# Performance work log

Hardware: AMD Instinct MI355X
Metric: run time of the kernel (lower is better)

## Reference

```python
import jax, jax.numpy as jnp
import numpy as np

Z, K, H, Y = 128, 256, 512, 4  # z_size, key_size, hidden_size, y_dim


def setup_inputs() -> dict:
    key = jax.random.key(0)
    ks = jax.random.split(key, 8)
    B, T, P = 512, 32, 32
    s = lambda k, shape, sc: (jax.random.normal(k, shape, jnp.float32) * sc)
    return {
        "x_seq": jax.random.normal(ks[0], (B, T, P, P), jnp.float32),
        "W_enc": s(ks[1], (P * P, Z), 0.03),
        "gamma": jnp.ones((Z,), jnp.float32),
        "beta": jnp.zeros((Z,), jnp.float32),
        "W_ih": s(ks[2], (4 * H, K + 1), 0.05),
        "W_hh": s(ks[3], (4 * H, H), 0.04),
        "b_ih": jnp.zeros((4 * H,), jnp.float32),
        "b_hh": jnp.zeros((4 * H,), jnp.float32),
        "W_key": s(ks[4], (K, H), 0.06),
        "b_key": jnp.zeros((K,), jnp.float32),
        "W_g": s(ks[5], (1, H), 0.06),
        "b_g": jnp.zeros((1,), jnp.float32),
        "conf_gain": jnp.ones((1,), jnp.float32),
        "conf_bias": jnp.zeros((1,), jnp.float32),
        "W_y": s(ks[6], (Y, H), 0.06),
        "b_y": jnp.zeros((Y,), jnp.float32),
    }


def _lstm_cell(x, h, c, W_ih, W_hh, b_ih, b_hh):
    # PyTorch gate order: i, f, g, o
    gates = x @ W_ih.T + b_ih + h @ W_hh.T + b_hh
    i, f, g, o = jnp.split(gates, 4, axis=-1)
    c = jax.nn.sigmoid(f) * c + jax.nn.sigmoid(i) * jnp.tanh(g)
    h = jax.nn.sigmoid(o) * jnp.tanh(c)
    return h, c


def _forward(x_seq, W_enc, gamma, beta, W_ih, W_hh, b_ih, b_hh,
             W_key, b_key, W_g, b_g, conf_gain, conf_bias, W_y, b_y):
    B, T, P, _ = x_seq.shape
    # encoder: flatten -> linear to z_size (stand-in for Encoder_mlp)
    z = x_seq.reshape(B, T, P * P) @ W_enc  # [B, T, Z]
    # context norm over the sequence dim (single task segment)
    mu = z.mean(axis=1, keepdims=True)
    sig = jnp.sqrt(z.var(axis=1, keepdims=True) + 1e-8)
    z = (z - mu) / sig * gamma + beta

    M = T + 1  # T+1 steps; final step feeds a zero z_t
    z_pad = jnp.concatenate([z, jnp.zeros((B, 1, Z), z.dtype)], axis=1)  # [B, M, Z]

    h0 = jnp.zeros((B, H), z.dtype)
    c0 = jnp.zeros((B, H), z.dtype)
    kr0 = jnp.zeros((B, K + 1), z.dtype)
    Mk0 = jnp.zeros((B, M, K), z.dtype)
    Mv0 = jnp.zeros((B, M, Z), z.dtype)

    def step(carry, t):
        h, c, key_r, M_k, M_v = carry
        z_t = jax.lax.dynamic_index_in_dim(z_pad, t, axis=1, keepdims=False)  # [B, Z]
        h, c = _lstm_cell(key_r, h, c, W_ih, W_hh, b_ih, b_hh)
        key_w = jax.nn.relu(h @ W_key.T + b_key)          # [B, K]
        g = jax.nn.sigmoid(h @ W_g.T + b_g)               # [B, 1]
        y_lin = h @ W_y.T + b_y                            # [B, Y]
        # attention read over valid memory slots j < t
        scores = jnp.einsum('bz,bmz->bm', z_t, M_v)        # [B, M]
        valid = (jnp.arange(M) < t)[None, :]
        w_k = jax.nn.softmax(jnp.where(valid, scores, -1e9), axis=1)
        c_k = jax.nn.sigmoid(scores * conf_gain + conf_bias)
        kv = jnp.concatenate([M_k, c_k[..., None]], axis=2)  # [B, M, K+1]
        attn = g * jnp.einsum('bm,bmd->bd', w_k, kv)          # [B, K+1]
        key_r_new = jnp.where(t == 0, jnp.zeros_like(attn), attn)
        # append to memory at slot t
        M_k = jax.lax.dynamic_update_slice_in_dim(M_k, key_w[:, None, :], t, axis=1)
        M_v = jax.lax.dynamic_update_slice_in_dim(M_v, z_t[:, None, :], t, axis=1)
        return (h, c, key_r_new, M_k, M_v), y_lin

    _, ys = jax.lax.scan(step, (h0, c0, kr0, Mk0, Mv0), jnp.arange(M))
    return ys[-1]  # y_pred_linear from final step, [B, Y]


def reference(x_seq, W_enc, gamma, beta, W_ih, W_hh, b_ih, b_hh,
              W_key, b_key, W_g, b_g, conf_gain, conf_bias, W_y, b_y):
    y_pred_linear = _forward(x_seq, W_enc, gamma, beta, W_ih, W_hh, b_ih, b_hh,
                             W_key, b_key, W_g, b_g, conf_gain, conf_bias, W_y, b_y)
    y_pred = jnp.argmax(y_pred_linear, axis=1)
    return y_pred_linear, y_pred
```

## Files before the change

kernel.cpp:

```cpp
#include <hip/hip_runtime.h>
#include <math.h>

typedef unsigned short ushort;
typedef unsigned int uint;
typedef __bf16 bf16x8 __attribute__((ext_vector_type(8)));
typedef float f32x4 __attribute__((ext_vector_type(4)));

#define ZS    128
#define KS    256
#define HS    512
#define BATCH 512
#define TT    32
#define MM    33
#define NB    2304
#define KPAD  800
#define HOFF  272
#define LDA   800

static __device__ __forceinline__ float sigf(float x) { return 1.f / (1.f + expf(-x)); }
static __device__ __forceinline__ float bf2f(ushort u) { return __uint_as_float((uint)u << 16); }

__global__ void prep_w(const float* __restrict__ W_ih, const float* __restrict__ W_hh,
                       const float* __restrict__ W_key, const float* __restrict__ b_ih,
                       const float* __restrict__ b_hh, const float* __restrict__ b_key,
                       const float* __restrict__ W_enc,
                       ushort* __restrict__ Whi, ushort* __restrict__ Wlo,
                       ushort* __restrict__ Behi, ushort* __restrict__ Belo,
                       float* __restrict__ biasN)
{
    int idx = blockIdx.x * 256 + threadIdx.x;
    if (idx < NB) {
        float bv;
        if (idx < 2048) { int j = idx >> 2, gi = idx & 3, r = gi * 512 + j; bv = b_ih[r] + b_hh[r]; }
        else bv = b_key[idx - 2048];
        biasN[idx] = bv;
    }
    if (idx < NB * KPAD) {
        int n = idx / KPAD, k = idx - n * KPAD;
        float v = 0.f;
        if (n < 2048) {
            int j = n >> 2, gi = n & 3, r = gi * 512 + j;
            if (k < 257) v = W_ih[r * 257 + k];
            else if (k >= HOFF && k < HOFF + 512) v = W_hh[r * 512 + (k - HOFF)];
        } else {
            if (k >= HOFF && k < HOFF + 512) v = W_key[(n - 2048) * 512 + (k - HOFF)];
        }
        uint u = __float_as_uint(v);
        Whi[idx] = (ushort)(u >> 16);
        float lo = v - __uint_as_float(u & 0xFFFF0000u);
        Wlo[idx] = (ushort)(__float_as_uint(lo) >> 16);
    } else if (idx < NB * KPAD + 128 * 1024) {
        int e = idx - NB * KPAD;
        int n = e >> 10, k = e & 1023;
        float v = W_enc[k * 128 + n];
        uint u = __float_as_uint(v);
        Behi[e] = (ushort)(u >> 16);
        float lo = v - __uint_as_float(u & 0xFFFF0000u);
        Belo[e] = (ushort)(__float_as_uint(lo) >> 16);
    }
}

__global__ __launch_bounds__(256, 4)
void gemm_enc(const float* __restrict__ A,
              const ushort* __restrict__ Bhi, const ushort* __restrict__ Blo,
              float* __restrict__ out)
{
    constexpr int BN = 128, NI = 4;
    constexpr int AHI = 0, ALO = 32 * 40, BHI = 64 * 40, BLO = 64 * 40 + BN * 40;
    constexpr int BUF = 64 * 40 + 2 * BN * 40;
    __shared__ ushort lds[2 * BUF];
    const int tid = threadIdx.x;
    const int row0 = blockIdx.x * 32, n0 = 0;
    const int lda = 1024, ldb = 1024, nslice = 32;
    const int l = tid & 63, w = tid >> 6, wm = w >> 1, wn = w & 1;
    const int lm = l & 15, kg = (l >> 4) << 3;

    f32x4 acc[NI];
    const f32x4 zero4 = {0.f, 0.f, 0.f, 0.f};
#pragma unroll
    for (int ni = 0; ni < NI; ni++) acc[ni] = zero4;

    float4 avf;
    uint4 bhv[BN / 64], blv[BN / 64];

    auto LOADG = [&](int s) {
        const int k0 = s * 32;
        int r = tid >> 3, c = (tid & 7) << 2;
        avf = *(const float4*)(A + (size_t)(row0 + r) * lda + k0 + c);
#pragma unroll
        for (int i = 0; i < BN / 64; i++) {
            int idx = tid + 256 * i, r2 = idx >> 2, c2 = (idx & 3) << 3;
            bhv[i] = *(const uint4*)(Bhi + (size_t)(n0 + r2) * ldb + k0 + c2);
            blv[i] = *(const uint4*)(Blo + (size_t)(n0 + r2) * ldb + k0 + c2);
        }
    };
    auto STORE = [&](int buf) {
        ushort* L = lds + buf * BUF;
        int r = tid >> 3, c = (tid & 7) << 2;
        uint u0 = __float_as_uint(avf.x), u1 = __float_as_uint(avf.y);
        uint u2 = __float_as_uint(avf.z), u3 = __float_as_uint(avf.w);
        uint hp0 = (u1 & 0xFFFF0000u) | (u0 >> 16);
        uint hp1 = (u3 & 0xFFFF0000u) | (u2 >> 16);
        float l0 = avf.x - __uint_as_float(u0 & 0xFFFF0000u);
        float l1 = avf.y - __uint_as_float(u1 & 0xFFFF0000u);
        float l2 = avf.z - __uint_as_float(u2 & 0xFFFF0000u);
        float l3 = avf.w - __uint_as_float(u3 & 0xFFFF0000u);
        uint lp0 = (__float_as_uint(l1) & 0xFFFF0000u) | (__float_as_uint(l0) >> 16);
        uint lp1 = (__float_as_uint(l3) & 0xFFFF0000u) | (__float_as_uint(l2) >> 16);
        *(uint2*)&L[AHI + r * 40 + c] = make_uint2(hp0, hp1);
        *(uint2*)&L[ALO + r * 40 + c] = make_uint2(lp0, lp1);
#pragma unroll
        for (int i = 0; i < BN / 64; i++) {
            int idx = tid + 256 * i, r2 = idx >> 2, c2 = (idx & 3) << 3;
            *(uint4*)&L[BHI + r2 * 40 + c2] = bhv[i];
            *(uint4*)&L[BLO + r2 * 40 + c2] = blv[i];
        }
    };
    auto COMPUTE = [&](int buf) {
        const ushort* L = lds + buf * BUF;
        bf16x8 ah, alv, bh[NI], bl[NI];
        {
            int r = wm * 16 + lm;
            ah  = *(const bf16x8*)&L[AHI + r * 40 + kg];
            alv = *(const bf16x8*)&L[ALO + r * 40 + kg];
        }
#pragma unroll
        for (int ni = 0; ni < NI; ni++) {
            int r = wn * (BN / 2) + ni * 16 + lm;
            bh[ni] = *(const bf16x8*)&L[BHI + r * 40 + kg];
            bl[ni] = *(const bf16x8*)&L[BLO + r * 40 + kg];
        }
#pragma unroll
        for (int ni = 0; ni < NI; ni++) {
            acc[ni] = __builtin_amdgcn_mfma_f32_16x16x32_bf16(ah,  bh[ni], acc[ni], 0, 0, 0);
            acc[ni] = __builtin_amdgcn_mfma_f32_16x16x32_bf16(ah,  bl[ni], acc[ni], 0, 0, 0);
            acc[ni] = __builtin_amdgcn_mfma_f32_16x16x32_bf16(alv, bh[ni], acc[ni], 0, 0, 0);
        }
    };

    LOADG(0);
    STORE(0);
    for (int s = 0; s < nslice; s++) {
        __syncthreads();
        if (s + 1 < nslice) LOADG(s + 1);
        COMPUTE(s & 1);
        if (s + 1 < nslice) STORE((s + 1) & 1);
    }

    const int crow = (l >> 4) << 2;
#pragma unroll
    for (int ni = 0; ni < NI; ni++)
#pragma unroll
        for (int r = 0; r < 4; r++) {
            int m = row0 + wm * 16 + crow + r;
            int z = n0 + wn * (BN / 2) + ni * 16 + lm;
            out[(size_t)(m >> 5) * (MM * ZS) + (m & 31) * ZS + z] = acc[ni][r];
        }
}

__global__ __launch_bounds__(256, 4)
void gemm_step(const ushort* __restrict__ Ahi, const ushort* __restrict__ Alo,
               const ushort* __restrict__ Whi, const ushort* __restrict__ Wlo,
               float* __restrict__ P0, float* __restrict__ P1)
{
    constexpr int AHI = 0, ALO = 64 * 40, BHI = 128 * 40, BLO = 192 * 40;
    constexpr int BUF = 256 * 40;
    __shared__ ushort lds[2 * BUF];
    const int tid = threadIdx.x;
    int wg = blockIdx.x;
    int swz = (wg & 7) * 72 + (wg >> 3);
    int zz = swz / 288;
    int rr = swz - zz * 288;
    const int bx = rr >> 3, by = rr & 7;
    const int kb = zz ? 13 : 0, kc = zz ? 12 : 13;
    float* __restrict__ out = zz ? P1 : P0;
    const int row0 = by * 64, n0 = bx * 64;
    const int l = tid & 63, w = tid >> 6, wm = w >> 1, wn = w & 1;
    const int lm = l & 15, kg = (l >> 4) << 3;
    const int ar = tid >> 2, ac = (tid & 3) << 3;

    f32x4 acc[2][2];
    const f32x4 zero4 = {0.f, 0.f, 0.f, 0.f};
    acc[0][0] = zero4; acc[0][1] = zero4; acc[1][0] = zero4; acc[1][1] = zero4;

    uint4 av0, av1, bv0, bv1;

    auto LOADG = [&](int a) {
        const int k0 = a * 32;
        av0 = *(const uint4*)(Ahi + (size_t)(row0 + ar) * LDA + k0 + ac);
        av1 = *(const uint4*)(Alo + (size_t)(row0 + ar) * LDA + k0 + ac);
        bv0 = *(const uint4*)(Whi + (size_t)(n0 + ar) * KPAD + k0 + ac);
        bv1 = *(const uint4*)(Wlo + (size_t)(n0 + ar) * KPAD + k0 + ac);
    };
    auto STORE = [&](int buf) {
        ushort* L = lds + buf * BUF;
        int off = ar * 40 + ac;
        *(uint4*)&L[AHI + off] = av0;
        *(uint4*)&L[ALO + off] = av1;
        *(uint4*)&L[BHI + off] = bv0;
        *(uint4*)&L[BLO + off] = bv1;
    };
    auto COMPUTE = [&](int buf) {
        const ushort* L = lds + buf * BUF;
        bf16x8 ah[2], al[2], bh[2], bl[2];
#pragma unroll
        for (int mi = 0; mi < 2; mi++) {
            int r = wm * 32 + mi * 16 + lm;
            ah[mi] = *(const bf16x8*)&L[AHI + r * 40 + kg];
            al[mi] = *(const bf16x8*)&L[ALO + r * 40 + kg];
        }
#pragma unroll
        for (int ni = 0; ni < 2; ni++) {
            int r = wn * 32 + ni * 16 + lm;
            bh[ni] = *(const bf16x8*)&L[BHI + r * 40 + kg];
            bl[ni] = *(const bf16x8*)&L[BLO + r * 40 + kg];
        }
#pragma unroll
        for (int mi = 0; mi < 2; mi++)
#pragma unroll
            for (int ni = 0; ni < 2; ni++) {
                acc[mi][ni] = __builtin_amdgcn_mfma_f32_16x16x32_bf16(ah[mi], bh[ni], acc[mi][ni], 0, 0, 0);
                acc[mi][ni] = __builtin_amdgcn_mfma_f32_16x16x32_bf16(ah[mi], bl[ni], acc[mi][ni], 0, 0, 0);
                acc[mi][ni] = __builtin_amdgcn_mfma_f32_16x16x32_bf16(al[mi], bh[ni], acc[mi][ni], 0, 0, 0);
            }
    };

    LOADG(kb);
    STORE(0);
    for (int s = 0; s < kc; s++) {
        __syncthreads();
        if (s + 1 < kc) LOADG(kb + s + 1);
        COMPUTE(s & 1);
        if (s + 1 < kc) STORE((s + 1) & 1);
    }

    const int crow = (l >> 4) << 2;
#pragma unroll
    for (int mi = 0; mi < 2; mi++)
#pragma unroll
        for (int ni = 0; ni < 2; ni++)
#pragma unroll
            for (int r = 0; r < 4; r++) {
                int b = row0 + wm * 32 + mi * 16 + crow + r;
                int n = n0 + wn * 32 + ni * 16 + lm;
                out[(size_t)b * NB + n] = acc[mi][ni][r];
            }
}

__global__ __launch_bounds__(256)
void cell_k(const float* __restrict__ P0, const float* __restrict__ P1,
            const float* __restrict__ biasN, float* __restrict__ cst,
            ushort* __restrict__ outHi, ushort* __restrict__ outLo,
            float* __restrict__ Mk,
            const float* __restrict__ W_g, const float* __restrict__ b_g,
            const float* __restrict__ watt, const float* __restrict__ wc,
            int t)
{
    __shared__ float hsh[512];
    __shared__ float red[256];
    __shared__ float wts[32];
    __shared__ float gsh;
    int b = blockIdx.x, tid = threadIdx.x;
    const float* p0 = P0 + (size_t)b * NB;
    const float* p1 = P1 + (size_t)b * NB;
    ushort* rHi = outHi + (size_t)b * LDA;
    ushort* rLo = outLo + (size_t)b * LDA;
#pragma unroll
    for (int u = 0; u < 2; u++) {
        int j = tid + u * 256;
        float4 a  = *(const float4*)(p0 + 4 * j);
        float4 c4 = *(const float4*)(p1 + 4 * j);
        float4 bb = *(const float4*)(biasN + 4 * j);
        float gi = a.x + c4.x + bb.x;
        float gf = a.y + c4.y + bb.y;
        float gg = a.z + c4.z + bb.z;
        float go = a.w + c4.w + bb.w;
        float iv = sigf(gi), fv = sigf(gf), gv = tanhf(gg), ov = sigf(go);
        float cn = fv * cst[(size_t)b * HS + j] + iv * gv;
        float hv = ov * tanhf(cn);
        cst[(size_t)b * HS + j] = cn;
        hsh[j] = hv;
        uint uu = __float_as_uint(hv);
        rHi[HOFF + j] = (ushort)(uu >> 16);
        float lo = hv - __uint_as_float(uu & 0xFFFF0000u);
        rLo[HOFF + j] = (ushort)(__float_as_uint(lo) >> 16);
    }
    float kv = fmaxf(p0[2048 + tid] + p1[2048 + tid] + biasN[2048 + tid], 0.f);
    if (t >= 1) Mk[((size_t)(t - 1) * BATCH + b) * KS + tid] = kv;
    if (t < 1 || t > 31) return;
    if (tid < t) wts[tid] = watt[(b * MM + t) * MM + tid];
    __syncthreads();
    red[tid] = hsh[tid] * W_g[tid] + hsh[tid + 256] * W_g[tid + 256];
    __syncthreads();
    for (int s = 128; s > 0; s >>= 1) {
        if (tid < s) red[tid] += red[tid + s];
        __syncthreads();
    }
    if (tid == 0) gsh = sigf(red[0] + b_g[0]);
    __syncthreads();
    float g = gsh;
    float acc = wts[t - 1] * kv;
    for (int m = 0; m < t - 1; m++)
        acc += wts[m] * Mk[((size_t)m * BATCH + b) * KS + tid];
    float v = g * acc;
    uint u2 = __float_as_uint(v);
    rHi[tid] = (ushort)(u2 >> 16);
    float lo2 = v - __uint_as_float(u2 & 0xFFFF0000u);
    rLo[tid] = (ushort)(__float_as_uint(lo2) >> 16);
    if (tid == 0) {
        float vc = g * wc[b * MM + t];
        uint uc = __float_as_uint(vc);
        rHi[256] = (ushort)(uc >> 16);
        float lc = vc - __uint_as_float(uc & 0xFFFF0000u);
        rLo[256] = (ushort)(__float_as_uint(lc) >> 16);
    }
}

__global__ void norm_k(float* __restrict__ z_pad, const float* __restrict__ gamma,
                       const float* __restrict__ beta)
{
    int b = blockIdx.x, zc = threadIdx.x;
    float* zb = z_pad + (size_t)b * (MM * ZS);
    float s = 0.f, s2 = 0.f;
    for (int t = 0; t < TT; t++) { float v = zb[t * ZS + zc]; s += v; s2 += v * v; }
    float mu = s * (1.f / 32.f);
    float var = s2 * (1.f / 32.f) - mu * mu;
    float rstd = 1.f / sqrtf(var + 1e-8f);
    float ga = gamma[zc], be = beta[zc];
    for (int t = 0; t < TT; t++) {
        float v = zb[t * ZS + zc];
        zb[t * ZS + zc] = (v - mu) * rstd * ga + be;
    }
    zb[TT * ZS + zc] = 0.f;
}

__global__ __launch_bounds__(256)
void scores_k(const float* __restrict__ z_pad, const float* __restrict__ cg_p,
              const float* __restrict__ cb_p, float* __restrict__ watt,
              float* __restrict__ wc)
{
    __shared__ float zs[MM * 129];
    int b = blockIdx.x, tid = threadIdx.x;
    const float* zb = z_pad + (size_t)b * (MM * ZS);
    for (int i = tid; i < MM * ZS; i += 256) {
        int m = i >> 7, k = i & 127;
        zs[m * 129 + k] = zb[i];
    }
    __syncthreads();
    float cg = cg_p[0], cb = cb_p[0];
    int wid = tid >> 6, lane = tid & 63;
    for (int t = 1 + wid; t <= 32; t += 4) {
        int m = lane;
        float s = -3.0e38f;
        if (m < t) {
            const float* zt = &zs[t * 129];
            const float* zm = &zs[m * 129];
            float acc = 0.f;
#pragma unroll 8
            for (int k = 0; k < ZS; k++) acc += zt[k] * zm[k];
            s = acc;
        }
        float mx = s;
        for (int off = 1; off < 64; off <<= 1) mx = fmaxf(mx, __shfl_xor(mx, off));
        float e = (m < t) ? expf(s - mx) : 0.f;
        float sum = e;
        for (int off = 1; off < 64; off <<= 1) sum += __shfl_xor(sum, off);
        float w = e / sum;
        if (m < t) watt[(b * MM + t) * MM + m] = w;
        float p = (m < t) ? w * sigf(s * cg + cb) : 0.f;
        for (int off = 1; off < 64; off <<= 1) p += __shfl_xor(p, off);
        if (lane == 0) wc[b * MM + t] = p;
    }
}

__global__ void y_k(const ushort* __restrict__ inpHi, const ushort* __restrict__ inpLo,
                    const float* __restrict__ W_y, const float* __restrict__ b_y,
                    float* __restrict__ out)
{
    int b = blockIdx.x, lane = threadIdx.x;
    const ushort* hHi = inpHi + (size_t)b * LDA + HOFF;
    const ushort* hLo = inpLo + (size_t)b * LDA + HOFF;
    float a0 = 0, a1 = 0, a2 = 0, a3 = 0;
    for (int r = 0; r < 8; r++) {
        int k = lane + r * 64;
        float hv = bf2f(hHi[k]) + bf2f(hLo[k]);
        a0 += hv * W_y[k];
        a1 += hv * W_y[512 + k];
        a2 += hv * W_y[1024 + k];
        a3 += hv * W_y[1536 + k];
    }
    for (int off = 32; off > 0; off >>= 1) {
        a0 += __shfl_xor(a0, off);
        a1 += __shfl_xor(a1, off);
        a2 += __shfl_xor(a2, off);
        a3 += __shfl_xor(a3, off);
    }
    if (lane == 0) {
        float y0 = a0 + b_y[0], y1 = a1 + b_y[1], y2 = a2 + b_y[2], y3 = a3 + b_y[3];
        out[b * 4 + 0] = y0; out[b * 4 + 1] = y1; out[b * 4 + 2] = y2; out[b * 4 + 3] = y3;
        int best = 0; float bv = y0;
        if (y1 > bv) { bv = y1; best = 1; }
        if (y2 > bv) { bv = y2; best = 2; }
        if (y3 > bv) { bv = y3; best = 3; }
        out[2048 + b] = (float)best;
    }
}

extern "C" void kernel_launch(void* const* d_in, const int* in_sizes, int n_in,
                              void* d_out, int out_size, void* d_ws, size_t ws_size,
                              hipStream_t stream)
{
    const float* x_seq = (const float*)d_in[0];
    const float* W_enc = (const float*)d_in[1];
    const float* gamma = (const float*)d_in[2];
    const float* beta  = (const float*)d_in[3];
    const float* W_ih  = (const float*)d_in[4];
    const float* W_hh  = (const float*)d_in[5];
    const float* b_ih  = (const float*)d_in[6];
    const float* b_hh  = (const float*)d_in[7];
    const float* W_key = (const float*)d_in[8];
    const float* b_key = (const float*)d_in[9];
    const float* W_g   = (const float*)d_in[10];
    const float* b_g   = (const float*)d_in[11];
    const float* cgain = (const float*)d_in[12];
    const float* cbias = (const float*)d_in[13];
    const float* W_y   = (const float*)d_in[14];
    const float* b_y   = (const float*)d_in[15];

    float* ws    = (float*)d_ws;
    float* z_pad = ws;
    float* watt  = z_pad + 2162688;
    float* wcv   = watt + 557568;
    float* Mk    = wcv + 16896;
    float* biasN = Mk + 4194304;
    float* cst   = biasN + 2304;
    ushort* inpHi0 = (ushort*)(cst + 262144);
    ushort* inpLo0 = inpHi0 + 409600;
    ushort* inpHi1 = inpLo0 + 409600;
    ushort* inpLo1 = inpHi1 + 409600;
    ushort* Whi  = inpLo1 + 409600;
    ushort* Wlo  = Whi + NB * KPAD;
    ushort* Behi = Wlo + NB * KPAD;
    ushort* Belo = Behi + 131072;
    float* P0 = (float*)(Belo + 131072);
    float* P1 = P0 + (size_t)BATCH * NB;

    hipMemsetAsync(cst, 0, 262144 * sizeof(float) + 4 * 409600 * sizeof(ushort), stream);

    prep_w<<<(NB * KPAD + 131072 + 255) / 256, 256, 0, stream>>>(
        W_ih, W_hh, W_key, b_ih, b_hh, b_key, W_enc, Whi, Wlo, Behi, Belo, biasN);

    gemm_enc<<<512, 256, 0, stream>>>(x_seq, Behi, Belo, z_pad);
    norm_k<<<512, 128, 0, stream>>>(z_pad, gamma, beta);
    scores_k<<<512, 256, 0, stream>>>(z_pad, cgain, cbias, watt, wcv);

    for (int t = 0; t <= 32; t++) {
        ushort* inHiC = (t & 1) ? inpHi1 : inpHi0;
        ushort* inLoC = (t & 1) ? inpLo1 : inpLo0;
        ushort* inHiN = (t & 1) ? inpHi0 : inpHi1;
        ushort* inLoN = (t & 1) ? inpLo0 : inpLo1;
        gemm_step<<<576, 256, 0, stream>>>(inHiC, inLoC, Whi, Wlo, P0, P1);
        cell_k<<<512, 256, 0, stream>>>(P0, P1, biasN, cst, inHiN, inLoN,
                                        Mk, W_g, b_g, watt, wcv, t);
    }
    y_k<<<512, 64, 0, stream>>>(inpHi1, inpLo1, W_y, b_y, (float*)d_out);
}
```

Baseline: 942.0 us.

## Fuse LSTM cell epilogue into per-step GEMM with single-wave 32x32 tiles

The per-step GEMM now uses one-wave 32x32 tiles that read operands straight from global memory, with no LDS staging and no split-K into P0/P1 partials. Its epilogue applies the bias and LSTM gate nonlinearities (or the ReLU key output) directly and writes h/c and the memory keys. A slimmer post kernel handles the gate scalar and the attention read, and it is skipped at steps where it does nothing. This removes the partial-sum round trip through global memory and part of each step's launch work, at the cost of losing LDS reuse and relying on cache hits for repeated operand loads. The post kernel rebuilds h from the hi/lo bf16 split rather than fp32, a small accuracy change.

```diff
diff --git a/kernel.cpp b/kernel.cpp
--- a/kernel.cpp
+++ b/kernel.cpp
@@ -158,63 +158,47 @@
         }
 }
 
-__global__ __launch_bounds__(256, 4)
+__global__ __launch_bounds__(64, 2)
 void gemm_step(const ushort* __restrict__ Ahi, const ushort* __restrict__ Alo,
                const ushort* __restrict__ Whi, const ushort* __restrict__ Wlo,
-               float* __restrict__ P0, float* __restrict__ P1)
-{
-    constexpr int AHI = 0, ALO = 64 * 40, BHI = 128 * 40, BLO = 192 * 40;
-    constexpr int BUF = 256 * 40;
-    __shared__ ushort lds[2 * BUF];
+               const float* __restrict__ biasN, float* __restrict__ cst,
+               ushort* __restrict__ outHi, ushort* __restrict__ outLo,
+               float* __restrict__ Mk, int t)
+{
+    __shared__ float eps[32 * 33];
     const int tid = threadIdx.x;
     int wg = blockIdx.x;
-    int swz = (wg & 7) * 72 + (wg >> 3);
-    int zz = swz / 288;
-    int rr = swz - zz * 288;
-    const int bx = rr >> 3, by = rr & 7;
-    const int kb = zz ? 13 : 0, kc = zz ? 12 : 13;
-    float* __restrict__ out = zz ? P1 : P0;
-    const int row0 = by * 64, n0 = bx * 64;
-    const int l = tid & 63, w = tid >> 6, wm = w >> 1, wn = w & 1;
-    const int lm = l & 15, kg = (l >> 4) << 3;
-    const int ar = tid >> 2, ac = (tid & 3) << 3;
+    int swz = (wg & 7) * 144 + (wg >> 3);
+    const int bx = swz >> 4, by = swz & 15;
+    const int row0 = by * 32, n0 = bx * 32;
+    const int lm = tid & 15, kg = (tid >> 4) << 3;
+    const int crow = (tid >> 4) << 2;
 
     f32x4 acc[2][2];
     const f32x4 zero4 = {0.f, 0.f, 0.f, 0.f};
     acc[0][0] = zero4; acc[0][1] = zero4; acc[1][0] = zero4; acc[1][1] = zero4;
 
-    uint4 av0, av1, bv0, bv1;
-
-    auto LOADG = [&](int a) {
-        const int k0 = a * 32;
-        av0 = *(const uint4*)(Ahi + (size_t)(row0 + ar) * LDA + k0 + ac);
-        av1 = *(const uint4*)(Alo + (size_t)(row0 + ar) * LDA + k0 + ac);
-        bv0 = *(const uint4*)(Whi + (size_t)(n0 + ar) * KPAD + k0 + ac);
-        bv1 = *(const uint4*)(Wlo + (size_t)(n0 + ar) * KPAD + k0 + ac);
-    };
-    auto STORE = [&](int buf) {
-        ushort* L = lds + buf * BUF;
-        int off = ar * 40 + ac;
-        *(uint4*)&L[AHI + off] = av0;
-        *(uint4*)&L[ALO + off] = av1;
-        *(uint4*)&L[BHI + off] = bv0;
-        *(uint4*)&L[BLO + off] = bv1;
-    };
-    auto COMPUTE = [&](int buf) {
-        const ushort* L = lds + buf * BUF;
+    const ushort* pA0h = Ahi + (size_t)(row0 + lm) * LDA + kg;
+    const ushort* pA1h = Ahi + (size_t)(row0 + 16 + lm) * LDA + kg;
+    const ushort* pA0l = Alo + (size_t)(row0 + lm) * LDA + kg;
+    const ushort* pA1l = Alo + (size_t)(row0 + 16 + lm) * LDA + kg;
+    const ushort* pB0h = Whi + (size_t)(n0 + lm) * KPAD + kg;
+    const ushort* pB1h = Whi + (size_t)(n0 + 16 + lm) * KPAD + kg;
+    const ushort* pB0l = Wlo + (size_t)(n0 + lm) * KPAD + kg;
+    const ushort* pB1l = Wlo + (size_t)(n0 + 16 + lm) * KPAD + kg;
+
+#pragma unroll
+    for (int s = 0; s < 25; s++) {
+        const int k0 = s * 32;
         bf16x8 ah[2], al[2], bh[2], bl[2];
-#pragma unroll
-        for (int mi = 0; mi < 2; mi++) {
-            int r = wm * 32 + mi * 16 + lm;
-            ah[mi] = *(const bf16x8*)&L[AHI + r * 40 + kg];
-            al[mi] = *(const bf16x8*)&L[ALO + r * 40 + kg];
-        }
-#pragma unroll
-        for (int ni = 0; ni < 2; ni++) {
-            int r = wn * 32 + ni * 16 + lm;
-            bh[ni] = *(const bf16x8*)&L[BHI + r * 40 + kg];
-            bl[ni] = *(const bf16x8*)&L[BLO + r * 40 + kg];
-        }
+        ah[0] = *(const bf16x8*)(pA0h + k0);
+        ah[1] = *(const bf16x8*)(pA1h + k0);
+        al[0] = *(const bf16x8*)(pA0l + k0);
+        al[1] = *(const bf16x8*)(pA1l + k0);
+        bh[0] = *(const bf16x8*)(pB0h + k0);
+        bh[1] = *(const bf16x8*)(pB1h + k0);
+        bl[0] = *(const bf16x8*)(pB0l + k0);
+        bl[1] = *(const bf16x8*)(pB1l + k0);
 #pragma unroll
         for (int mi = 0; mi < 2; mi++)
 #pragma unroll
@@ -223,74 +207,69 @@
                 acc[mi][ni] = __builtin_amdgcn_mfma_f32_16x16x32_bf16(ah[mi], bl[ni], acc[mi][ni], 0, 0, 0);
                 acc[mi][ni] = __builtin_amdgcn_mfma_f32_16x16x32_bf16(al[mi], bh[ni], acc[mi][ni], 0, 0, 0);
             }
-    };
-
-    LOADG(kb);
-    STORE(0);
-    for (int s = 0; s < kc; s++) {
+    }
+
+    if (n0 < 2048) {
+#pragma unroll
+        for (int mi = 0; mi < 2; mi++)
+#pragma unroll
+            for (int ni = 0; ni < 2; ni++)
+#pragma unroll
+                for (int r = 0; r < 4; r++) {
+                    int ml = mi * 16 + crow + r, cl = ni * 16 + lm;
+                    eps[ml * 33 + cl] = acc[mi][ni][r] + biasN[n0 + cl];
+                }
         __syncthreads();
-        if (s + 1 < kc) LOADG(kb + s + 1);
-        COMPUTE(s & 1);
-        if (s + 1 < kc) STORE((s + 1) & 1);
-    }
-
-    const int crow = (l >> 4) << 2;
-#pragma unroll
-    for (int mi = 0; mi < 2; mi++)
-#pragma unroll
-        for (int ni = 0; ni < 2; ni++)
-#pragma unroll
-            for (int r = 0; r < 4; r++) {
-                int b = row0 + wm * 32 + mi * 16 + crow + r;
-                int n = n0 + wn * 32 + ni * 16 + lm;
-                out[(size_t)b * NB + n] = acc[mi][ni][r];
-            }
+        int u = tid & 7, rg = tid >> 3;
+        int j = (n0 >> 2) + u;
+#pragma unroll
+        for (int q = 0; q < 4; q++) {
+            int r2 = rg * 4 + q;
+            int b = row0 + r2;
+            float gi = eps[r2 * 33 + u * 4 + 0];
+            float gf = eps[r2 * 33 + u * 4 + 1];
+            float gg = eps[r2 * 33 + u * 4 + 2];
+            float go = eps[r2 * 33 + u * 4 + 3];
+            float iv = sigf(gi), fv = sigf(gf), gv = tanhf(gg), ov = sigf(go);
+            float cn = fv * cst[(size_t)b * HS + j] + iv * gv;
+            float hv = ov * tanhf(cn);
+            cst[(size_t)b * HS + j] = cn;
+            uint uu = __float_as_uint(hv);
+            outHi[(size_t)b * LDA + HOFF + j] = (ushort)(uu >> 16);
+            float lo = hv - __uint_as_float(uu & 0xFFFF0000u);
+            outLo[(size_t)b * LDA + HOFF + j] = (ushort)(__float_as_uint(lo) >> 16);
+        }
+    } else if (t >= 1) {
+#pragma unroll
+        for (int mi = 0; mi < 2; mi++)
+#pragma unroll
+            for (int ni = 0; ni < 2; ni++)
+#pragma unroll
+                for (int r = 0; r < 4; r++) {
+                    int b = row0 + mi * 16 + crow + r;
+                    int cg = n0 + ni * 16 + lm;
+                    float v = fmaxf(acc[mi][ni][r] + biasN[cg], 0.f);
+                    Mk[((size_t)(t - 1) * BATCH + b) * KS + (cg - 2048)] = v;
+                }
+    }
 }
 
 __global__ __launch_bounds__(256)
-void cell_k(const float* __restrict__ P0, const float* __restrict__ P1,
-            const float* __restrict__ biasN, float* __restrict__ cst,
-            ushort* __restrict__ outHi, ushort* __restrict__ outLo,
-            float* __restrict__ Mk,
+void post_k(ushort* __restrict__ inpHi, ushort* __restrict__ inpLo,
             const float* __restrict__ W_g, const float* __restrict__ b_g,
             const float* __restrict__ watt, const float* __restrict__ wc,
-            int t)
-{
-    __shared__ float hsh[512];
+            const float* __restrict__ Mk, int t)
+{
     __shared__ float red[256];
     __shared__ float wts[32];
     __shared__ float gsh;
     int b = blockIdx.x, tid = threadIdx.x;
-    const float* p0 = P0 + (size_t)b * NB;
-    const float* p1 = P1 + (size_t)b * NB;
-    ushort* rHi = outHi + (size_t)b * LDA;
-    ushort* rLo = outLo + (size_t)b * LDA;
-#pragma unroll
-    for (int u = 0; u < 2; u++) {
-        int j = tid + u * 256;
-        float4 a  = *(const float4*)(p0 + 4 * j);
-        float4 c4 = *(const float4*)(p1 + 4 * j);
-        float4 bb = *(const float4*)(biasN + 4 * j);
-        float gi = a.x + c4.x + bb.x;
-        float gf = a.y + c4.y + bb.y;
-        float gg = a.z + c4.z + bb.z;
-        float go = a.w + c4.w + bb.w;
-        float iv = sigf(gi), fv = sigf(gf), gv = tanhf(gg), ov = sigf(go);
-        float cn = fv * cst[(size_t)b * HS + j] + iv * gv;
-        float hv = ov * tanhf(cn);
-        cst[(size_t)b * HS + j] = cn;
-        hsh[j] = hv;
-        uint uu = __float_as_uint(hv);
-        rHi[HOFF + j] = (ushort)(uu >> 16);
-        float lo = hv - __uint_as_float(uu & 0xFFFF0000u);
-        rLo[HOFF + j] = (ushort)(__float_as_uint(lo) >> 16);
-    }
-    float kv = fmaxf(p0[2048 + tid] + p1[2048 + tid] + biasN[2048 + tid], 0.f);
-    if (t >= 1) Mk[((size_t)(t - 1) * BATCH + b) * KS + tid] = kv;
-    if (t < 1 || t > 31) return;
+    ushort* rHi = inpHi + (size_t)b * LDA;
+    ushort* rLo = inpLo + (size_t)b * LDA;
+    float h1 = bf2f(rHi[HOFF + tid]) + bf2f(rLo[HOFF + tid]);
+    float h2 = bf2f(rHi[HOFF + 256 + tid]) + bf2f(rLo[HOFF + 256 + tid]);
+    red[tid] = h1 * W_g[tid] + h2 * W_g[tid + 256];
     if (tid < t) wts[tid] = watt[(b * MM + t) * MM + tid];
-    __syncthreads();
-    red[tid] = hsh[tid] * W_g[tid] + hsh[tid + 256] * W_g[tid + 256];
     __syncthreads();
     for (int s = 128; s > 0; s >>= 1) {
         if (tid < s) red[tid] += red[tid + s];
@@ -299,14 +278,14 @@
     if (tid == 0) gsh = sigf(red[0] + b_g[0]);
     __syncthreads();
     float g = gsh;
-    float acc = wts[t - 1] * kv;
-    for (int m = 0; m < t - 1; m++)
+    float acc = 0.f;
+    for (int m = 0; m < t; m++)
         acc += wts[m] * Mk[((size_t)m * BATCH + b) * KS + tid];
     float v = g * acc;
-    uint u2 = __float_as_uint(v);
-    rHi[tid] = (ushort)(u2 >> 16);
-    float lo2 = v - __uint_as_float(u2 & 0xFFFF0000u);
-    rLo[tid] = (ushort)(__float_as_uint(lo2) >> 16);
+    uint u = __float_as_uint(v);
+    rHi[tid] = (ushort)(u >> 16);
+    float lo = v - __uint_as_float(u & 0xFFFF0000u);
+    rLo[tid] = (ushort)(__float_as_uint(lo) >> 16);
     if (tid == 0) {
         float vc = g * wc[b * MM + t];
         uint uc = __float_as_uint(vc);
@@ -442,8 +421,6 @@
     ushort* Wlo  = Whi + NB * KPAD;
     ushort* Behi = Wlo + NB * KPAD;
     ushort* Belo = Behi + 131072;
-    float* P0 = (float*)(Belo + 131072);
-    float* P1 = P0 + (size_t)BATCH * NB;
 
     hipMemsetAsync(cst, 0, 262144 * sizeof(float) + 4 * 409600 * sizeof(ushort), stream);
 
@@ -459,9 +436,10 @@
         ushort* inLoC = (t & 1) ? inpLo1 : inpLo0;
         ushort* inHiN = (t & 1) ? inpHi0 : inpHi1;
         ushort* inLoN = (t & 1) ? inpLo0 : inpLo1;
-        gemm_step<<<576, 256, 0, stream>>>(inHiC, inLoC, Whi, Wlo, P0, P1);
-        cell_k<<<512, 256, 0, stream>>>(P0, P1, biasN, cst, inHiN, inLoN,
-                                        Mk, W_g, b_g, watt, wcv, t);
+        gemm_step<<<1152, 64, 0, stream>>>(inHiC, inLoC, Whi, Wlo, biasN, cst,
+                                           inHiN, inLoN, Mk, t);
+        if (t >= 1 && t <= 31)
+            post_k<<<512, 256, 0, stream>>>(inHiN, inLoN, W_g, b_g, watt, wcv, Mk, t);
     }
     y_k<<<512, 64, 0, stream>>>(inpHi1, inpLo1, W_y, b_y, (float*)d_out);
 }
```

After: 1.214 ms. +28.9%, slower.
